# Kernel optimization log

Measured on AMD Instinct MI355X. Metric: run time of the kernel, lower is better.

Reference implementation:

```python
import jax, jax.numpy as jnp
import numpy as np

DEPTH = 3
DIM = 64
N_NODES = 4096
BATCH = 4


def setup_inputs() -> dict:
    key = jax.random.key(0)
    k1, k2, k3, k4 = jax.random.split(key, 4)
    x = jax.random.normal(k1, (BATCH, N_NODES, DIM), dtype=jnp.float32)
    graph = jax.random.uniform(k2, (BATCH, N_NODES, N_NODES), dtype=jnp.float32)
    # Linear((depth+1)*dim, dim): PyTorch default init U(-1/sqrt(fan_in), 1/sqrt(fan_in))
    fan_in = (DEPTH + 1) * DIM
    bound = 1.0 / np.sqrt(fan_in)
    W = jax.random.uniform(k3, (DIM, fan_in), minval=-bound, maxval=bound, dtype=jnp.float32)
    b = jax.random.uniform(k4, (DIM,), minval=-bound, maxval=bound, dtype=jnp.float32)
    return {"x": x, "graph": graph, "W": W, "b": b}


def reference(x, graph, W, b):
    # GCN branch of LocalGNN.forward (dropout p=0 -> identity).
    n = graph.shape[-1]
    g = graph + jnp.eye(n, dtype=graph.dtype)          # add self loops
    d = 1.0 / (jnp.sqrt(g.sum(axis=-1)) + 1e-7)        # [b, n]
    # D @ g @ D with D = diag(d):  g_ij * d_i * d_j
    g = g * d[..., :, None] * d[..., None, :]
    outs = [x]
    h = x
    for _ in range(DEPTH):
        h = jnp.einsum('bij,bjd->bid', g, h)           # dense propagation
        outs.append(h)
    cat = jnp.concatenate(outs, axis=-1)               # [b, n, (depth+1)*dim]
    return cat @ W.T + b
```

## Files before the change

### kernel.cpp

```cpp
#include <hip/hip_runtime.h>
#include <hip/hip_bf16.h>


typedef __attribute__((ext_vector_type(4))) float  floatx4;
typedef __attribute__((ext_vector_type(8))) short  short8;

#define NB 4
#define NN 4096
#define ND 64
#define HF_B 262144

__device__ __forceinline__ unsigned short f2bf_bits(float v) {
    __hip_bfloat16 b = __float2bfloat16(v);
    return *reinterpret_cast<unsigned short*>(&b);
}
__device__ __forceinline__ float bf2f(unsigned short u) {
    unsigned int x = ((unsigned int)u) << 16;
    return *reinterpret_cast<float*>(&x);
}
__device__ __forceinline__ short8 pack8p(const float* v) {
    short8 r;
#pragma unroll
    for (int j = 0; j < 8; ++j) r[j] = (short)f2bf_bits(v[j]);
    return r;
}

#define PREP_LOAD(DST, CH)                                              \
    _Pragma("unroll")                                                   \
    for (int gg = 0; gg < 4; ++gg) {                                    \
        int kb = (CH) * 512 + (gg * 4 + w) * 32 + q * 8;                \
        DST[2 * gg]     = *reinterpret_cast<const floatx4*>(rowp + kb); \
        DST[2 * gg + 1] = *reinterpret_cast<const floatx4*>(rowp + kb + 4); \
    }
#define PREP_PROC(SRC, CH)                                              \
    _Pragma("unroll")                                                   \
    for (int gg = 0; gg < 4; ++gg) {                                    \
        int kcl = gg * 4 + w;                                           \
        int kbase = (CH) * 512 + kcl * 32 + q * 8;                      \
        float v[8];                                                     \
        _Pragma("unroll")                                               \
        for (int j = 0; j < 8; ++j) {                                   \
            float xv = (j < 4) ? SRC[2 * gg][j] : SRC[2 * gg + 1][j - 4]; \
            rs += xv;                                \
            v[j] = xv + ((kbase + j == i_row) ? 1.0f : 0.0f);    \
        }                                                               \
        *reinterpret_cast<short8*>(gswz + outbase + ((size_t)((CH) * 16 + kcl)) * 512 + (size_t)lane * 8) = pack8p(v); \
    }

__global__ __launch_bounds__(256, 4) void prep_graph(const float* __restrict__ g,
                                                     const float* __restrict__ x,
                                                     const float* __restrict__ W,
                                                     float* __restrict__ dinv,
                                                     unsigned short* __restrict__ gswz,
                                                     unsigned short* __restrict__ hF0,
                                                     unsigned short* __restrict__ Wf) {
    __shared__ float rsum[4][16];
    __shared__ float dl[16];
    int tt = blockIdx.x;
    int b = tt >> 8, mt = tt & 255;
    int t = threadIdx.x;
    int w = t >> 6, lane = t & 63;
    int m = lane & 15, q = lane >> 4;
    const float* rowp = g + ((size_t)b * NN + mt * 16 + m) * NN;
    size_t outbase = (size_t)tt * 128 * 512;
    int i_row = mt * 16 + m;
    float rs = 0.f;
    floatx4 bufA[8], bufB[8];

    PREP_LOAD(bufA, 0)
    PREP_LOAD(bufB, 1) PREP_PROC(bufA, 0)
    PREP_LOAD(bufA, 2) PREP_PROC(bufB, 1)
    PREP_LOAD(bufB, 3) PREP_PROC(bufA, 2)
    PREP_LOAD(bufA, 4) PREP_PROC(bufB, 3)
    PREP_LOAD(bufB, 5) PREP_PROC(bufA, 4)
    PREP_LOAD(bufA, 6) PREP_PROC(bufB, 5)
    PREP_LOAD(bufB, 7) PREP_PROC(bufA, 6)
    PREP_PROC(bufB, 7)

    rs += __shfl_xor(rs, 16);
    rs += __shfl_xor(rs, 32);
    if (lane < 16) rsum[w][lane] = rs;
    __syncthreads();
    if (t < 16) {
        float tot = rsum[0][t] + rsum[1][t] + rsum[2][t] + rsum[3][t];
        float d = 1.0f / (sqrtf(tot + 1.0f) + 1e-7f);
        dinv[b * NN + mt * 16 + t] = d;
        dl[t] = d;
    }
    __syncthreads();
    if (t < 128) {
        int c = t >> 5, lnl = t & 31;
        int q_loc = lnl >> 4, mm = lnl & 15;
        int u = mt & 1, kc2 = mt >> 1;
        int ln = u * 32 + lnl;
        const float* xp = x + ((size_t)b * NN + mt * 16) * ND + c * 16 + mm;
        float v[8];
#pragma unroll
        for (int j = 0; j < 8; ++j) {
            int lr = q_loc * 8 + j;
            v[j] = dl[lr] * xp[(size_t)lr * ND];
        }
        *reinterpret_cast<short8*>(hF0 + (size_t)b * HF_B + ((size_t)(kc2 * 4 + c) * 64 + ln) * 8) = pack8p(v);
    }
    if (tt == 0) {
#pragma unroll
        for (int e = 0; e < 8; ++e) {
            int wi = e * 256 + t;
            int kc2 = wi >> 8;
            int c = (wi >> 6) & 3;
            int ln = wi & 63;
            int mm = ln & 15, qq = ln >> 4;
            float v[8];
#pragma unroll
            for (int j = 0; j < 8; ++j) v[j] = W[(size_t)(c * 16 + mm) * 256 + kc2 * 32 + qq * 8 + j];
            *reinterpret_cast<short8*>(Wf + ((size_t)(kc2 * 4 + c) * 64 + ln) * 8) = pack8p(v);
        }
    }
}

#define PROP_MAIN()                                                                      \
    int bid = blockIdx.x;                                                                \
    int b = bid >> 8, mk = bid & 255;                                                    \
    int t = threadIdx.x;                                                                 \
    int w = t >> 6, lane = t & 63;                                                       \
    int m = lane & 15, q = lane >> 4;                                                    \
    const unsigned short* Ap = gswz + ((size_t)(b * 256 + mk) * 128 + w * 32) * 512 + (size_t)lane * 8; \
    const unsigned short* Bp = hFin + (size_t)b * HF_B + (size_t)(w * 32) * 2048 + (size_t)lane * 8;    \
    floatx4 acc[4];                                                                      \
    _Pragma("unroll")                                                                    \
    for (int c = 0; c < 4; ++c) acc[c] = (floatx4){0.f, 0.f, 0.f, 0.f};                  \
    _Pragma("unroll")                                                                    \
    for (int kc = 0; kc < 32; ++kc) {                                                    \
        size_t ao = (size_t)kc * 512, bo = (size_t)kc * 2048;                            \
        short8 a0 = *reinterpret_cast<const short8*>(Ap + ao);                           \
        short8 b0 = *reinterpret_cast<const short8*>(Bp + bo);                           \
        short8 b1 = *reinterpret_cast<const short8*>(Bp + bo + 512);                     \
        short8 b2 = *reinterpret_cast<const short8*>(Bp + bo + 1024);                    \
        short8 b3 = *reinterpret_cast<const short8*>(Bp + bo + 1536);                    \
        acc[0] = __builtin_amdgcn_mfma_f32_16x16x32_bf16(a0, b0, acc[0], 0, 0, 0);       \
        acc[1] = __builtin_amdgcn_mfma_f32_16x16x32_bf16(a0, b1, acc[1], 0, 0, 0);       \
        acc[2] = __builtin_amdgcn_mfma_f32_16x16x32_bf16(a0, b2, acc[2], 0, 0, 0);       \
        acc[3] = __builtin_amdgcn_mfma_f32_16x16x32_bf16(a0, b3, acc[3], 0, 0, 0);       \
    }                                                                                    \
    if (t < 16) dl[t] = dinv[b * NN + mk * 16 + t];                                      \
    _Pragma("unroll")                                                                    \
    for (int c = 0; c < 4; ++c)                                                          \
        _Pragma("unroll")                                                                \
        for (int r = 0; r < 4; ++r) buf[w][q * 4 + r][c * 16 + m] = acc[c][r];           \
    __syncthreads();                                                                     \
    _Pragma("unroll")                                                                    \
    for (int e = 0; e < 4; ++e) {                                                        \
        int idx = e * 256 + t;                                                           \
        int r = idx >> 6, col = idx & 63;                                                \
        float s = buf[0][r][col] + buf[1][r][col] + buf[2][r][col] + buf[3][r][col];     \
        hsh[r][col] = f2bf_bits(dl[r] * s);                                              \
    }                                                                                    \
    __syncthreads();

__global__ __launch_bounds__(256, 4) void prop_pass(const unsigned short* __restrict__ gswz,
                                                    const unsigned short* __restrict__ hFin,
                                                    const float* __restrict__ dinv,
                                                    unsigned short* __restrict__ hrow,
                                                    unsigned short* __restrict__ hFout) {
    __shared__ float buf[4][16][68];
    __shared__ unsigned short hsh[16][64];
    __shared__ float dl[16];
    PROP_MAIN()
    {
        unsigned short* hp = hrow + ((size_t)b * NN + mk * 16) * ND;
#pragma unroll
        for (int e = 0; e < 4; ++e) {
            int idx = e * 256 + t;
            hp[idx] = hsh[idx >> 6][idx & 63];
        }
    }
    if (t < 128) {
        int c = t >> 5, lnl = t & 31;
        int q_loc = lnl >> 4, mm = lnl & 15;
        int u = mk & 1, kc2 = mk >> 1;
        int ln = u * 32 + lnl;
        float v[8];
#pragma unroll
        for (int j = 0; j < 8; ++j) {
            int lr = q_loc * 8 + j;
            v[j] = dl[lr] * bf2f(hsh[lr][c * 16 + mm]);
        }
        *reinterpret_cast<short8*>(hFout + (size_t)b * HF_B + ((size_t)(kc2 * 4 + c) * 64 + ln) * 8) = pack8p(v);
    }
}

__global__ __launch_bounds__(256, 4) void prop_final(const unsigned short* __restrict__ gswz,
                                                     const unsigned short* __restrict__ hFin,
                                                     const float* __restrict__ dinv,
                                                     const float* __restrict__ x,
                                                     const unsigned short* __restrict__ hrow1,
                                                     const unsigned short* __restrict__ hrow2,
                                                     const unsigned short* __restrict__ Wf,
                                                     const float* __restrict__ bias,
                                                     float* __restrict__ out) {
    __shared__ float buf[4][16][68];
    __shared__ unsigned short hsh[16][64];
    __shared__ float dl[16];
    PROP_MAIN()
    {
        int grow_r = b * NN + mk * 16 + m;
        floatx4 facc = (floatx4){0.f, 0.f, 0.f, 0.f};
#pragma unroll
        for (int p = 0; p < 4; ++p) {
#pragma unroll
            for (int ki = 0; ki < 2; ++ki) {
                short8 af;
                if (p == 0) {
                    const float* xp = x + (size_t)grow_r * ND + ki * 32 + q * 8;
                    float v[8];
#pragma unroll
                    for (int j = 0; j < 8; ++j) v[j] = xp[j];
                    af = pack8p(v);
                } else if (p == 1) {
                    af = *reinterpret_cast<const short8*>(hrow1 + (size_t)grow_r * ND + ki * 32 + q * 8);
                } else if (p == 2) {
                    af = *reinterpret_cast<const short8*>(hrow2 + (size_t)grow_r * ND + ki * 32 + q * 8);
                } else {
                    af = *reinterpret_cast<const short8*>(&hsh[m][ki * 32 + q * 8]);
                }
                int kc2 = p * 2 + ki;
                short8 bf = *reinterpret_cast<const short8*>(Wf + ((size_t)(kc2 * 4 + w) * 64 + lane) * 8);
                facc = __builtin_amdgcn_mfma_f32_16x16x32_bf16(af, bf, facc, 0, 0, 0);
            }
        }
        float bb = bias[w * 16 + m];
#pragma unroll
        for (int r = 0; r < 4; ++r) {
            int row = b * NN + mk * 16 + q * 4 + r;
            out[(size_t)row * ND + w * 16 + m] = facc[r] + bb;
        }
    }
}

extern "C" void kernel_launch(void* const* d_in, const int* in_sizes, int n_in,
                              void* d_out, int out_size, void* d_ws, size_t ws_size,
                              hipStream_t stream) {
    const float* x     = (const float*)d_in[0];
    const float* graph = (const float*)d_in[1];
    const float* W     = (const float*)d_in[2];
    const float* bias  = (const float*)d_in[3];
    float* out = (float*)d_out;

    char* wsp = (char*)d_ws;
    float*          dinv  = (float*)wsp;
    unsigned short* Wf    = (unsigned short*)(wsp + (1 << 16));
    unsigned short* hFa   = (unsigned short*)(wsp + (1 << 17));
    unsigned short* hFb   = hFa + (size_t)NB * HF_B;
    unsigned short* hrow1 = hFb + (size_t)NB * HF_B;
    unsigned short* hrow2 = hrow1 + (size_t)NB * NN * ND;
    unsigned short* gswz  = hrow2 + (size_t)NB * NN * ND;

    prep_graph<<<1024, 256, 0, stream>>>(graph, x, W, dinv, gswz, hFa, Wf);
    prop_pass<<<1024, 256, 0, stream>>>(gswz, hFa, dinv, hrow1, hFb);
    prop_pass<<<1024, 256, 0, stream>>>(gswz, hFb, dinv, hrow2, hFa);
    prop_final<<<1024, 256, 0, stream>>>(gswz, hFa, dinv, x, hrow1, hrow2, Wf, bias, out);
}
```

Measured before the change: 491.2 us.

## Double-buffer propagation operands through LDS with async global_load_lds

The propagation GEMM main loop now uses global_load_lds to stream A and B fragments into a per-wave double-buffered LDS slot. It issues two stages ahead and uses explicit vmcnt/lgkmcnt waits, so global memory latency overlaps the MFMA work. The shared memory is merged into one aliased buffer, which adds a barrier before the reduction reuses it. This raises LDS use to 40KB per block and adds extra LDS round trips, which may limit occupancy.

Result: no change. 489.4 us (-0.4%).

```diff
diff --git a/kernel.cpp b/kernel.cpp
--- a/kernel.cpp
+++ b/kernel.cpp
@@ -23,6 +23,12 @@
 #pragma unroll
     for (int j = 0; j < 8; ++j) r[j] = (short)f2bf_bits(v[j]);
     return r;
+}
+
+__device__ __forceinline__ void gld16(const unsigned short* g, unsigned short* l) {
+    __builtin_amdgcn_global_load_lds(
+        (const __attribute__((address_space(1))) unsigned int*)g,
+        (__attribute__((address_space(3))) unsigned int*)l, 16, 0, 0);
 }
 
 #define PREP_LOAD(DST, CH)                                              \
@@ -118,31 +124,57 @@
     }
 }
 
-#define PROP_MAIN()                                                                      \
+#define PSTAGE(S, P) {                                                                   \
+    int kk_ = w * 32 + (S);                                                              \
+    unsigned short* sl_ = slotb + (P) * 2560;                                            \
+    const unsigned short* ga_ = gA + (size_t)kk_ * 512 + lane * 8;                       \
+    const unsigned short* gb_ = gB + (size_t)kk_ * 2048 + lane * 8;                      \
+    gld16(ga_, sl_);                                                                     \
+    gld16(gb_, sl_ + 512);                                                               \
+    gld16(gb_ + 512, sl_ + 1024);                                                        \
+    gld16(gb_ + 1024, sl_ + 1536);                                                       \
+    gld16(gb_ + 1536, sl_ + 2048);                                                       \
+}
+
+#define PROP_MAIN(HFIN)                                                                  \
     int bid = blockIdx.x;                                                                \
     int b = bid >> 8, mk = bid & 255;                                                    \
     int t = threadIdx.x;                                                                 \
     int w = t >> 6, lane = t & 63;                                                       \
     int m = lane & 15, q = lane >> 4;                                                    \
-    const unsigned short* Ap = gswz + ((size_t)(b * 256 + mk) * 128 + w * 32) * 512 + (size_t)lane * 8; \
-    const unsigned short* Bp = hFin + (size_t)b * HF_B + (size_t)(w * 32) * 2048 + (size_t)lane * 8;    \
+    float dv = 0.f;                                                                      \
+    if (t < 16) dv = dinv[b * NN + mk * 16 + t];     \
+    unsigned short* smem_us = (unsigned short*)smemf;                                    \
+    float (*buf)[16][68] = (float (*)[16][68])smemf;         \
+    unsigned short* hshp = (unsigned short*)(smemf + 4352);                  \
+    float* dlp = smemf + 4352 + 512;                                           \
+    const unsigned short* gA = gswz + (size_t)(b * 256 + mk) * 128 * 512;                \
+    const unsigned short* gB = (HFIN) + (size_t)b * HF_B;                                \
+    unsigned short* slotb = smem_us + w * 5120;                                          \
     floatx4 acc[4];                                                                      \
     _Pragma("unroll")                                                                    \
     for (int c = 0; c < 4; ++c) acc[c] = (floatx4){0.f, 0.f, 0.f, 0.f};                  \
-    _Pragma("unroll")                                                                    \
-    for (int kc = 0; kc < 32; ++kc) {                                                    \
-        size_t ao = (size_t)kc * 512, bo = (size_t)kc * 2048;                            \
-        short8 a0 = *reinterpret_cast<const short8*>(Ap + ao);                           \
-        short8 b0 = *reinterpret_cast<const short8*>(Bp + bo);                           \
-        short8 b1 = *reinterpret_cast<const short8*>(Bp + bo + 512);                     \
-        short8 b2 = *reinterpret_cast<const short8*>(Bp + bo + 1024);                    \
-        short8 b3 = *reinterpret_cast<const short8*>(Bp + bo + 1536);                    \
+    PSTAGE(0, 0)                                                                         \
+    PSTAGE(1, 1)                                                                         \
+    _Pragma("unroll")                                                                    \
+    for (int s = 0; s < 32; ++s) {                                                       \
+        if (s < 31) { asm volatile("s_waitcnt vmcnt(5)" ::: "memory"); }                 \
+        else        { asm volatile("s_waitcnt vmcnt(0)" ::: "memory"); }                 \
+        const unsigned short* sl = slotb + (s & 1) * 2560;                               \
+        short8 a0 = *reinterpret_cast<const short8*>(sl + lane * 8);                     \
+        short8 b0 = *reinterpret_cast<const short8*>(sl + 512 + lane * 8);               \
+        short8 b1 = *reinterpret_cast<const short8*>(sl + 1024 + lane * 8);              \
+        short8 b2 = *reinterpret_cast<const short8*>(sl + 1536 + lane * 8);              \
+        short8 b3 = *reinterpret_cast<const short8*>(sl + 2048 + lane * 8);              \
+        asm volatile("s_waitcnt lgkmcnt(0)" ::: "memory");   \
+        if (s < 30) PSTAGE(s + 2, s & 1)                                                 \
         acc[0] = __builtin_amdgcn_mfma_f32_16x16x32_bf16(a0, b0, acc[0], 0, 0, 0);       \
         acc[1] = __builtin_amdgcn_mfma_f32_16x16x32_bf16(a0, b1, acc[1], 0, 0, 0);       \
         acc[2] = __builtin_amdgcn_mfma_f32_16x16x32_bf16(a0, b2, acc[2], 0, 0, 0);       \
         acc[3] = __builtin_amdgcn_mfma_f32_16x16x32_bf16(a0, b3, acc[3], 0, 0, 0);       \
     }                                                                                    \
-    if (t < 16) dl[t] = dinv[b * NN + mk * 16 + t];                                      \
+    __syncthreads();                                \
+    if (t < 16) dlp[t] = dv;                                                             \
     _Pragma("unroll")                                                                    \
     for (int c = 0; c < 4; ++c)                                                          \
         _Pragma("unroll")                                                                \
@@ -152,8 +184,8 @@
     for (int e = 0; e < 4; ++e) {                                                        \
         int idx = e * 256 + t;                                                           \
         int r = idx >> 6, col = idx & 63;                                                \
-        float s = buf[0][r][col] + buf[1][r][col] + buf[2][r][col] + buf[3][r][col];     \
-        hsh[r][col] = f2bf_bits(dl[r] * s);                                              \
+        float sv = buf[0][r][col] + buf[1][r][col] + buf[2][r][col] + buf[3][r][col];    \
+        hshp[r * 64 + col] = f2bf_bits(dlp[r] * sv);                                     \
     }                                                                                    \
     __syncthreads();
 
@@ -162,16 +194,14 @@
                                                     const float* __restrict__ dinv,
                                                     unsigned short* __restrict__ hrow,
                                                     unsigned short* __restrict__ hFout) {
-    __shared__ float buf[4][16][68];
-    __shared__ unsigned short hsh[16][64];
-    __shared__ float dl[16];
-    PROP_MAIN()
+    __shared__ float smemf[10240];
+    PROP_MAIN(hFin)
     {
         unsigned short* hp = hrow + ((size_t)b * NN + mk * 16) * ND;
 #pragma unroll
         for (int e = 0; e < 4; ++e) {
             int idx = e * 256 + t;
-            hp[idx] = hsh[idx >> 6][idx & 63];
+            hp[idx] = hshp[idx];
         }
     }
     if (t < 128) {
@@ -183,7 +213,7 @@
 #pragma unroll
         for (int j = 0; j < 8; ++j) {
             int lr = q_loc * 8 + j;
-            v[j] = dl[lr] * bf2f(hsh[lr][c * 16 + mm]);
+            v[j] = dlp[lr] * bf2f(hshp[lr * 64 + c * 16 + mm]);
         }
         *reinterpret_cast<short8*>(hFout + (size_t)b * HF_B + ((size_t)(kc2 * 4 + c) * 64 + ln) * 8) = pack8p(v);
     }
@@ -198,10 +228,8 @@
                                                      const unsigned short* __restrict__ Wf,
                                                      const float* __restrict__ bias,
                                                      float* __restrict__ out) {
-    __shared__ float buf[4][16][68];
-    __shared__ unsigned short hsh[16][64];
-    __shared__ float dl[16];
-    PROP_MAIN()
+    __shared__ float smemf[10240];
+    PROP_MAIN(hFin)
     {
         int grow_r = b * NN + mk * 16 + m;
         floatx4 facc = (floatx4){0.f, 0.f, 0.f, 0.f};
@@ -221,7 +249,7 @@
                 } else if (p == 2) {
                     af = *reinterpret_cast<const short8*>(hrow2 + (size_t)grow_r * ND + ki * 32 + q * 8);
                 } else {
-                    af = *reinterpret_cast<const short8*>(&hsh[m][ki * 32 + q * 8]);
+                    af = *reinterpret_cast<const short8*>(&hshp[m * 64 + ki * 32 + q * 8]);
                 }
                 int kc2 = p * 2 + ki;
                 short8 bf = *reinterpret_cast<const short8*>(Wf + ((size_t)(kc2 * 4 + w) * 64 + lane) * 8);
```

## Process two 16-row tiles per block to reuse h fragments, remap block ids

Applied to the files above, without the earlier changes.

Each propagation block now computes 32 output rows (two 16-row tiles) instead of 16, so every B-fragment load of h feeds two MFMAs. This halves the h-operand traffic per graph element and halves the grid to 512 blocks. A block-id permutation spreads the batches across XCDs/CUs. The per-tile reduction through shared memory is looped, and the final projection is done by two waves each covering all 64 output columns. The cost is higher register pressure from doubled accumulators and fewer blocks, which lowers parallelism.

Result: no change. 483.3 us (-1.6%).

```diff
diff --git a/kernel.cpp b/kernel.cpp
--- a/kernel.cpp
+++ b/kernel.cpp
@@ -119,41 +119,54 @@
 }
 
 #define PROP_MAIN()                                                                      \
-    int bid = blockIdx.x;                                                                \
-    int b = bid >> 8, mk = bid & 255;                                                    \
+    int bid0 = blockIdx.x;                                                               \
+    int lid = ((bid0 & 7) << 6) + (bid0 >> 3);                  \
+    int b = lid >> 7, mk = lid & 127;                                                    \
     int t = threadIdx.x;                                                                 \
     int w = t >> 6, lane = t & 63;                                                       \
     int m = lane & 15, q = lane >> 4;                                                    \
-    const unsigned short* Ap = gswz + ((size_t)(b * 256 + mk) * 128 + w * 32) * 512 + (size_t)lane * 8; \
-    const unsigned short* Bp = hFin + (size_t)b * HF_B + (size_t)(w * 32) * 2048 + (size_t)lane * 8;    \
-    floatx4 acc[4];                                                                      \
+    int tt0 = b * 256 + mk * 2;                                                          \
+    const unsigned short* Ap0 = gswz + ((size_t)tt0 * 128 + w * 32) * 512 + (size_t)lane * 8; \
+    const unsigned short* Ap1 = Ap0 + (size_t)128 * 512;                                 \
+    const unsigned short* Bp  = hFin + (size_t)b * HF_B + (size_t)(w * 32) * 2048 + (size_t)lane * 8; \
+    floatx4 acc0[4], acc1[4];                                                            \
     _Pragma("unroll")                                                                    \
-    for (int c = 0; c < 4; ++c) acc[c] = (floatx4){0.f, 0.f, 0.f, 0.f};                  \
+    for (int c = 0; c < 4; ++c) { acc0[c] = (floatx4){0.f,0.f,0.f,0.f}; acc1[c] = acc0[c]; } \
     _Pragma("unroll")                                                                    \
     for (int kc = 0; kc < 32; ++kc) {                                                    \
         size_t ao = (size_t)kc * 512, bo = (size_t)kc * 2048;                            \
-        short8 a0 = *reinterpret_cast<const short8*>(Ap + ao);                           \
+        short8 a0 = *reinterpret_cast<const short8*>(Ap0 + ao);                          \
+        short8 a1 = *reinterpret_cast<const short8*>(Ap1 + ao);                          \
         short8 b0 = *reinterpret_cast<const short8*>(Bp + bo);                           \
         short8 b1 = *reinterpret_cast<const short8*>(Bp + bo + 512);                     \
         short8 b2 = *reinterpret_cast<const short8*>(Bp + bo + 1024);                    \
         short8 b3 = *reinterpret_cast<const short8*>(Bp + bo + 1536);                    \
-        acc[0] = __builtin_amdgcn_mfma_f32_16x16x32_bf16(a0, b0, acc[0], 0, 0, 0);       \
-        acc[1] = __builtin_amdgcn_mfma_f32_16x16x32_bf16(a0, b1, acc[1], 0, 0, 0);       \
-        acc[2] = __builtin_amdgcn_mfma_f32_16x16x32_bf16(a0, b2, acc[2], 0, 0, 0);       \
-        acc[3] = __builtin_amdgcn_mfma_f32_16x16x32_bf16(a0, b3, acc[3], 0, 0, 0);       \
+        acc0[0] = __builtin_amdgcn_mfma_f32_16x16x32_bf16(a0, b0, acc0[0], 0, 0, 0);     \
+        acc1[0] = __builtin_amdgcn_mfma_f32_16x16x32_bf16(a1, b0, acc1[0], 0, 0, 0);     \
+        acc0[1] = __builtin_amdgcn_mfma_f32_16x16x32_bf16(a0, b1, acc0[1], 0, 0, 0);     \
+        acc1[1] = __builtin_amdgcn_mfma_f32_16x16x32_bf16(a1, b1, acc1[1], 0, 0, 0);     \
+        acc0[2] = __builtin_amdgcn_mfma_f32_16x16x32_bf16(a0, b2, acc0[2], 0, 0, 0);     \
+        acc1[2] = __builtin_amdgcn_mfma_f32_16x16x32_bf16(a1, b2, acc1[2], 0, 0, 0);     \
+        acc0[3] = __builtin_amdgcn_mfma_f32_16x16x32_bf16(a0, b3, acc0[3], 0, 0, 0);     \
+        acc1[3] = __builtin_amdgcn_mfma_f32_16x16x32_bf16(a1, b3, acc1[3], 0, 0, 0);     \
     }                                                                                    \
-    if (t < 16) dl[t] = dinv[b * NN + mk * 16 + t];                                      \
-    _Pragma("unroll")                                                                    \
-    for (int c = 0; c < 4; ++c)                                                          \
+    if (t < 32) dl[t] = dinv[b * NN + mk * 32 + t];                                      \
+    for (int u = 0; u < 2; ++u) {                                                        \
+        __syncthreads();                                                                 \
+        floatx4* acc = u ? acc1 : acc0;                                                  \
         _Pragma("unroll")                                                                \
-        for (int r = 0; r < 4; ++r) buf[w][q * 4 + r][c * 16 + m] = acc[c][r];           \
-    __syncthreads();                                                                     \
-    _Pragma("unroll")                                                                    \
-    for (int e = 0; e < 4; ++e) {                                                        \
-        int idx = e * 256 + t;                                                           \
-        int r = idx >> 6, col = idx & 63;                                                \
-        float s = buf[0][r][col] + buf[1][r][col] + buf[2][r][col] + buf[3][r][col];     \
-        hsh[r][col] = f2bf_bits(dl[r] * s);                                              \
+        for (int c = 0; c < 4; ++c)                                                      \
+            _Pragma("unroll")                                                            \
+            for (int r = 0; r < 4; ++r) buf[w][q * 4 + r][c * 16 + m] = acc[c][r];       \
+        __syncthreads();                                                                 \
+        _Pragma("unroll")                                                                \
+        for (int e = 0; e < 4; ++e) {                                                    \
+            int idx = e * 256 + t;                                                       \
+            int r = idx >> 6, col = idx & 63;                                            \
+            float s = buf[0][r][col] + buf[1][r][col] + buf[2][r][col] + buf[3][r][col]; \
+            int lr = u * 16 + r;                                                         \
+            hsh[lr][col] = f2bf_bits(dl[lr] * s);                                        \
+        }                                                                                \
     }                                                                                    \
     __syncthreads();
 
@@ -163,29 +176,27 @@
                                                     unsigned short* __restrict__ hrow,
                                                     unsigned short* __restrict__ hFout) {
     __shared__ float buf[4][16][68];
-    __shared__ unsigned short hsh[16][64];
-    __shared__ float dl[16];
+    __shared__ unsigned short hsh[32][64];
+    __shared__ float dl[32];
     PROP_MAIN()
     {
-        unsigned short* hp = hrow + ((size_t)b * NN + mk * 16) * ND;
-#pragma unroll
-        for (int e = 0; e < 4; ++e) {
+        unsigned short* hp = hrow + ((size_t)b * NN + mk * 32) * ND;
+#pragma unroll
+        for (int e = 0; e < 8; ++e) {
             int idx = e * 256 + t;
             hp[idx] = hsh[idx >> 6][idx & 63];
         }
     }
-    if (t < 128) {
-        int c = t >> 5, lnl = t & 31;
-        int q_loc = lnl >> 4, mm = lnl & 15;
-        int u = mk & 1, kc2 = mk >> 1;
-        int ln = u * 32 + lnl;
+    {
+        int c = t >> 6, ln = t & 63;
+        int mm = ln & 15, qq = ln >> 4;
         float v[8];
 #pragma unroll
         for (int j = 0; j < 8; ++j) {
-            int lr = q_loc * 8 + j;
+            int lr = qq * 8 + j;
             v[j] = dl[lr] * bf2f(hsh[lr][c * 16 + mm]);
         }
-        *reinterpret_cast<short8*>(hFout + (size_t)b * HF_B + ((size_t)(kc2 * 4 + c) * 64 + ln) * 8) = pack8p(v);
+        *reinterpret_cast<short8*>(hFout + (size_t)b * HF_B + ((size_t)(mk * 4 + c) * 64 + ln) * 8) = pack8p(v);
     }
 }
 
@@ -199,40 +210,49 @@
                                                      const float* __restrict__ bias,
                                                      float* __restrict__ out) {
     __shared__ float buf[4][16][68];
-    __shared__ unsigned short hsh[16][64];
-    __shared__ float dl[16];
+    __shared__ unsigned short hsh[32][64];
+    __shared__ float dl[32];
     PROP_MAIN()
-    {
-        int grow_r = b * NN + mk * 16 + m;
-        floatx4 facc = (floatx4){0.f, 0.f, 0.f, 0.f};
+    if (w < 2) {
+        int u = w;
+        int grow = b * NN + mk * 32 + u * 16 + m;
+        floatx4 facc[4];
+#pragma unroll
+        for (int c = 0; c < 4; ++c) facc[c] = (floatx4){0.f, 0.f, 0.f, 0.f};
 #pragma unroll
         for (int p = 0; p < 4; ++p) {
 #pragma unroll
             for (int ki = 0; ki < 2; ++ki) {
                 short8 af;
                 if (p == 0) {
-                    const float* xp = x + (size_t)grow_r * ND + ki * 32 + q * 8;
+                    const float* xp = x + (size_t)grow * ND + ki * 32 + q * 8;
                     float v[8];
 #pragma unroll
                     for (int j = 0; j < 8; ++j) v[j] = xp[j];
                     af = pack8p(v);
                 } else if (p == 1) {
-                    af = *reinterpret_cast<const short8*>(hrow1 + (size_t)grow_r * ND + ki * 32 + q * 8);
+                    af = *reinterpret_cast<const short8*>(hrow1 + (size_t)grow * ND + ki * 32 + q * 8);
                 } else if (p == 2) {
-                    af = *reinterpret_cast<const short8*>(hrow2 + (size_t)grow_r * ND + ki * 32 + q * 8);
+                    af = *reinterpret_cast<const short8*>(hrow2 + (size_t)grow * ND + ki * 32 + q * 8);
                 } else {
-                    af = *reinterpret_cast<const short8*>(&hsh[m][ki * 32 + q * 8]);
+                    af = *reinterpret_cast<const short8*>(&hsh[u * 16 + m][ki * 32 + q * 8]);
                 }
-                int kc2 = p * 2 + ki;
-                short8 bf = *reinterpret_cast<const short8*>(Wf + ((size_t)(kc2 * 4 + w) * 64 + lane) * 8);
-                facc = __builtin_amdgcn_mfma_f32_16x16x32_bf16(af, bf, facc, 0, 0, 0);
+                int kc = p * 2 + ki;
+#pragma unroll
+                for (int c = 0; c < 4; ++c) {
+                    short8 bf = *reinterpret_cast<const short8*>(Wf + ((size_t)(kc * 4 + c) * 64 + lane) * 8);
+                    facc[c] = __builtin_amdgcn_mfma_f32_16x16x32_bf16(af, bf, facc[c], 0, 0, 0);
+                }
             }
         }
-        float bb = bias[w * 16 + m];
-#pragma unroll
-        for (int r = 0; r < 4; ++r) {
-            int row = b * NN + mk * 16 + q * 4 + r;
-            out[(size_t)row * ND + w * 16 + m] = facc[r] + bb;
+#pragma unroll
+        for (int c = 0; c < 4; ++c) {
+            float bb = bias[c * 16 + m];
+#pragma unroll
+            for (int r = 0; r < 4; ++r) {
+                int row = b * NN + mk * 32 + u * 16 + q * 4 + r;
+                out[(size_t)row * ND + c * 16 + m] = facc[c][r] + bb;
+            }
         }
     }
 }
@@ -256,7 +276,7 @@
     unsigned short* gswz  = hrow2 + (size_t)NB * NN * ND;
 
     prep_graph<<<1024, 256, 0, stream>>>(graph, x, W, dinv, gswz, hFa, Wf);
-    prop_pass<<<1024, 256, 0, stream>>>(gswz, hFa, dinv, hrow1, hFb);
-    prop_pass<<<1024, 256, 0, stream>>>(gswz, hFb, dinv, hrow2, hFa);
-    prop_final<<<1024, 256, 0, stream>>>(gswz, hFa, dinv, x, hrow1, hrow2, Wf, bias, out);
-}
+    prop_pass<<<512, 256, 0, stream>>>(gswz, hFa, dinv, hrow1, hFb);
+    prop_pass<<<512, 256, 0, stream>>>(gswz, hFb, dinv, hrow2, hFa);
+    prop_final<<<512, 256, 0, stream>>>(gswz, hFa, dinv, x, hrow1, hrow2, Wf, bias, out);
+}
```
